# Performance work log

Measured on AMD Instinct MI355X. Metric: run time of the kernel, lower is better.

## Reference

```python
import jax, jax.numpy as jnp
import numpy as np

N, S, D, H = 2048, 16, 128, 8
EPS = 1e-5  # torch.nn.LayerNorm default eps


def setup_inputs() -> dict:
    key = jax.random.key(0)
    ks = jax.random.split(key, 3)
    return {
        "x": jax.random.normal(ks[0], (N, S, D), jnp.float32),
        "Wi": jax.random.normal(ks[1], (H, S, D, D), jnp.float32),
        "Wj": jax.random.normal(ks[2], (H, S, 2 * D, D), jnp.float32),
        "ln1_w": jnp.ones((S, D), jnp.float32),
        "ln1_b": jnp.zeros((S, D), jnp.float32),
        "prelu1_a": jnp.float32(0.25),  # torch PReLU default single param
        "ln2_w": jnp.ones((H, D), jnp.float32),
        "ln2_b": jnp.zeros((H, D), jnp.float32),
        "prelu2_a": jnp.float32(0.25),
    }


def _layernorm2(x, w, b):
    # LayerNorm over the last two dims (matches torch LayerNorm([A, B]))
    mu = jnp.mean(x, axis=(-2, -1), keepdims=True)
    var = jnp.var(x, axis=(-2, -1), keepdims=True)
    return (x - mu) * jax.lax.rsqrt(var + EPS) * w + b


def _prelu(x, a):
    return jnp.where(x >= 0, x, a * x)


def reference(x, Wi, Wj, ln1_w, ln1_b, prelu1_a, ln2_w, ln2_b, prelu2_a):
    n, s, d = x.shape
    h = Wi.shape[0]
    # sort descending along source dim
    idx = jnp.argsort(-x, axis=1)                      # [N,S,D] int
    x_sort = jnp.take_along_axis(x, idx, axis=1)       # [N,S,D]
    # pad with a zero row, take adjacent differences
    pad = jnp.concatenate([x_sort, jnp.zeros((n, 1, d), x.dtype)], axis=1)
    diff = pad[:, :-1, :] - pad[:, 1:, :]              # [N,S,D]
    # positional encoding: cumsum of 2^rank / 2^S
    enc = jnp.cumsum(jnp.exp2(idx.astype(x.dtype)), axis=1) / jnp.asarray(2.0 ** s, x.dtype)
    # per-head, per-source batched matmul with Wi
    se = jnp.einsum('bsd,hsdo->bhso', enc, Wi)         # [N,H,S,D]
    se = _prelu(_layernorm2(se, ln1_w, ln1_b), prelu1_a)  # Dropout in eval mode = identity
    cat = jnp.concatenate(
        [jnp.broadcast_to(diff[:, None, :, :], (n, h, s, d)), se], axis=-1
    )                                                  # [N,H,S,2D]
    out = jnp.einsum('bhsd,hsdo->bho', cat, Wj)        # [N,H,D]
    return _prelu(_layernorm2(out, ln2_w, ln2_b), prelu2_a)
```

## Files before the change

kernel.cpp:

```cpp
#include <hip/hip_runtime.h>

#define N_ 2048
#define S_ 16
#define D_ 128
#define H_ 8
#define EPS_ 1e-5f

typedef unsigned short ushortT;
typedef unsigned int uint32;
typedef __attribute__((ext_vector_type(8))) short short8;
typedef __attribute__((ext_vector_type(8))) unsigned short ushort8;
typedef __attribute__((ext_vector_type(4))) float f32x4;
typedef __attribute__((ext_vector_type(4))) unsigned int uint4v;
typedef __attribute__((ext_vector_type(8))) float float8;

__device__ __forceinline__ ushortT f2bf(float f) {
  union { float f; uint32 u; } c; c.f = f;
  uint32 u = c.u;
  u = (u + 0x7FFFu + ((u >> 16) & 1u)) >> 16;
  return (ushortT)u;
}
__device__ __forceinline__ float bf2f(ushortT b) {
  union { uint32 u; float f; } c; c.u = ((uint32)b) << 16;
  return c.f;
}

__global__ __launch_bounds__(256) void k_prep(const float* __restrict__ x,
                                              ushortT* __restrict__ enc_sw,
                                              ushortT* __restrict__ diff_sw) {
  int g = blockIdx.x * 256 + threadIdx.x;
  int n = g >> 7, d = g & 127;
  const float* xp = x + (size_t)n * (S_ * D_) + d;
  float v[S_];
#pragma unroll
  for (int s = 0; s < S_; ++s) v[s] = xp[s * D_];
  int r[S_];
#pragma unroll
  for (int i = 0; i < S_; ++i) {
    int ri = 0;
#pragma unroll
    for (int j = 0; j < S_; ++j)
      ri += ((v[j] > v[i]) || (v[j] == v[i] && j < i)) ? 1 : 0;
    r[i] = ri;
  }
  float xs[S_ + 1];
#pragma unroll
  for (int s = 0; s < S_; ++s) {
    float acc = 0.f;
#pragma unroll
    for (int i = 0; i < S_; ++i) acc += (r[i] == s) ? v[i] : 0.f;
    xs[s] = acc;
  }
  xs[S_] = 0.f;
  int btq = n >> 7, row = n & 127;
  int wv = row >> 5, ii = (row >> 4) & 1, l = row & 15;
  int kkm = d >> 5, lgm = (d >> 3) & 3, em = d & 7;
  int off_nd = (((kkm * 2 + ii) * 64) + (lgm * 16 + l)) * 8 + em;
  int pp = d >> 6, c8p = (d >> 3) & 7, ee = d & 7;
  int q = row * 8 + (c8p ^ (row & 7));
#pragma unroll
  for (int s = 0; s < S_; ++s) {
    uint32 mm = 0;
#pragma unroll
    for (int i = 0; i < S_; ++i) mm |= (r[i] <= s) ? (1u << i) : 0u;
    enc_sw[(size_t)((btq * 16 + s) * 4 + wv) * 4096 + off_nd] =
        f2bf((float)mm * (1.f / 65536.f));
    size_t idx = ((((size_t)(btq * 16 + s) * 2 + pp) * 1024) + q) * 8 + ee;
    diff_sw[idx] = f2bf(xs[s] - xs[s + 1]);
  }
}

__global__ __launch_bounds__(256) void k_castW(const float* __restrict__ Wi,
                                               const float* __restrict__ Wj,
                                               ushortT* __restrict__ Wit_sw,
                                               ushortT* __restrict__ Wjt_sw) {
  __shared__ ushortT tile[128 * 136];
  int bx = blockIdx.x;
  int t = threadIdx.x;
  if (bx < 128) {
    int hs = bx;
    const float* src = Wi + (size_t)hs * D_ * D_;
#pragma unroll 4
    for (int i = 0; i < 64; ++i) {
      int e = t + 256 * i;
      int dd = e >> 7, o = e & 127;
      tile[dd * 136 + o] = f2bf(src[e]);
    }
    __syncthreads();
    ushortT* dst = Wit_sw + (size_t)hs * 16384;
#pragma unroll
    for (int r8 = 0; r8 < 8; ++r8) {
      int qc = r8 * 256 + t;
      int o = qc >> 4;
      int cc = (qc & 15) ^ (o & 7);
      uint4v pk;
#pragma unroll
      for (int w = 0; w < 4; ++w) {
        int d0 = cc * 8 + w * 2;
        ushortT lo = tile[d0 * 136 + o];
        ushortT hi = tile[(d0 + 1) * 136 + o];
        pk[w] = (uint32)lo | ((uint32)hi << 16);
      }
      *(uint4v*)(dst + qc * 8) = pk;
    }
  } else {
    int hs = bx - 128;
    const float* src = Wj + (size_t)hs * 256 * D_;
    for (int half = 0; half < 2; ++half) {
      if (half) __syncthreads();
#pragma unroll 4
      for (int i = 0; i < 64; ++i) {
        int e = t + 256 * i;
        int dd = e >> 7, o = e & 127;
        tile[dd * 136 + o] = f2bf(src[half * 16384 + e]);
      }
      __syncthreads();
      ushortT* dstb = Wjt_sw + ((size_t)hs * 4 + half * 2) * 8192;
#pragma unroll
      for (int r8 = 0; r8 < 8; ++r8) {
        int cg = r8 * 256 + t;
        int pl = cg >> 10;
        int qc = cg & 1023;
        int o = qc >> 3;
        int c8 = (qc & 7) ^ (o & 7);
        int dl = pl * 64 + c8 * 8;
        uint4v pk;
#pragma unroll
        for (int w = 0; w < 4; ++w) {
          ushortT lo = tile[(dl + w * 2) * 136 + o];
          ushortT hi = tile[(dl + w * 2 + 1) * 136 + o];
          pk[w] = (uint32)lo | ((uint32)hi << 16);
        }
        *(uint4v*)(dstb + (size_t)pl * 8192 + qc * 8) = pk;
      }
    }
  }
}

__global__ __launch_bounds__(256, 3) void k_gemm1(const ushortT* __restrict__ enc_sw,
                                                  const ushortT* __restrict__ Wit_sw,
                                                  ushortT* __restrict__ se,
                                                  float* __restrict__ ssum,
                                                  float* __restrict__ ssq) {
  int bt = blockIdx.x, s = blockIdx.y, h = blockIdx.z;
  __shared__ ushortT Bs[128 * 132];
  int tid = threadIdx.x;
  int wave = tid >> 6, lane = tid & 63;
  int l15 = lane & 15, lg = lane >> 4;

  const ushortT* bsrc = Wit_sw + (size_t)(h * 16 + s) * 16384;
#pragma unroll
  for (int r8 = 0; r8 < 8; ++r8)
    __builtin_amdgcn_global_load_lds(
        (const __attribute__((address_space(1))) void*)(bsrc + (r8 * 256 + tid) * 8),
        (__attribute__((address_space(3))) void*)(Bs + (r8 * 256 + wave * 64) * 8),
        16, 0, 0);

  short8 afr[4][2];
  const ushortT* abase = enc_sw + ((size_t)(bt * 16 + s) * 4 + wave) * 4096;
#pragma unroll
  for (int kk = 0; kk < 4; ++kk)
#pragma unroll
    for (int i = 0; i < 2; ++i)
      afr[kk][i] = *(const short8*)(abase + ((kk * 2 + i) * 64 + lane) * 8);

  __syncthreads();

  f32x4 acc[2][8];
#pragma unroll
  for (int i = 0; i < 2; ++i)
#pragma unroll
    for (int j = 0; j < 8; ++j) acc[i][j] = (f32x4)(0.f);
#pragma unroll
  for (int kk = 0; kk < 4; ++kk) {
    int cc = kk * 4 + lg;
    short8 b[8];
#pragma unroll
    for (int j = 0; j < 8; ++j) {
      int row = j * 16 + l15;
      b[j] = *(const short8*)(Bs + (row * 16 + (cc ^ (row & 7))) * 8);
    }
#pragma unroll
    for (int i = 0; i < 2; ++i)
#pragma unroll
      for (int j = 0; j < 8; ++j)
        acc[i][j] = __builtin_amdgcn_mfma_f32_16x16x32_bf16(afr[kk][i], b[j], acc[i][j], 0, 0, 0);
  }
#pragma unroll
  for (int i = 0; i < 2; ++i)
#pragma unroll
    for (int rr = 0; rr < 4; ++rr) {
      int rloc = wave * 32 + i * 16 + lg * 4 + rr;
      int b_g = bt * 128 + rloc;
      float rs = 0.f, rq = 0.f;
#pragma unroll
      for (int j = 0; j < 8; ++j) {
        float val = acc[i][j][rr];
        rs += val; rq += val * val;
      }
#pragma unroll
      for (int m = 1; m <= 8; m <<= 1) {
        rs += __shfl_xor(rs, m);
        rq += __shfl_xor(rq, m);
      }
      if (l15 == 0) {
        ssum[((size_t)s * N_ + b_g) * H_ + h] = rs;
        ssq[((size_t)s * N_ + b_g) * H_ + h] = rq;
      }
    }
  __syncthreads();
#pragma unroll
  for (int i = 0; i < 2; ++i)
#pragma unroll
    for (int rr = 0; rr < 4; ++rr) {
      int row = wave * 32 + i * 16 + lg * 4 + rr;
      int sw = (row & 7) << 3;
#pragma unroll
      for (int j = 0; j < 8; ++j) {
        int o = j * 16 + l15;
        Bs[row * 132 + (o ^ sw)] = f2bf(acc[i][j][rr]);
      }
    }
  __syncthreads();
#pragma unroll
  for (int p = 0; p < 2; ++p) {
    int row = p * 64 + (tid >> 2);
    int sw = (row & 7) << 3;
    int b_g = bt * 128 + row;
    ushortT* dst = se + (((size_t)b_g * H_ + h) * S_ + s) * D_;
#pragma unroll
    for (int qq = 0; qq < 4; ++qq) {
      int o0 = (qq * 4 + (tid & 3)) * 8;
      *(uint4v*)(dst + o0) = *(const uint4v*)(Bs + row * 132 + (o0 ^ sw));
    }
  }
}

__global__ __launch_bounds__(256) void k_finalize(const float* __restrict__ ssum,
                                                  const float* __restrict__ ssq,
                                                  float* __restrict__ mr) {
  int t = blockIdx.x * 256 + threadIdx.x;
  float s1 = 0.f, s2 = 0.f;
#pragma unroll
  for (int s = 0; s < S_; ++s) {
    s1 += ssum[(size_t)s * (N_ * H_) + t];
    s2 += ssq[(size_t)s * (N_ * H_) + t];
  }
  float mu = s1 * (1.f / 2048.f);
  float var = s2 * (1.f / 2048.f) - mu * mu;
  float rstd = rsqrtf(var + EPS_);
  mr[t * 2] = rstd;
  mr[t * 2 + 1] = -mu * rstd;
}

#define GLDS_TILE(DST, SRC) do {                                              \
    const ushortT* sp_ = (SRC) + wave * 512 + lane * 8;                       \
    ushortT* dp_ = (DST) + wave * 512;                                        \
    _Pragma("unroll")                                                         \
    for (int i_ = 0; i_ < 4; ++i_)                                            \
      __builtin_amdgcn_global_load_lds(                                       \
          (const __attribute__((address_space(1))) void*)(sp_ + i_ * 2048),   \
          (__attribute__((address_space(3))) void*)(dp_ + i_ * 2048),         \
          16, 0, 0);                                                          \
  } while (0)

__global__ __launch_bounds__(256, 2) void k_gemm2(const ushortT* __restrict__ diff_sw,
                                                  const ushortT* __restrict__ se,
                                                  const ushortT* __restrict__ Wjt_sw,
                                                  const float* __restrict__ mr,
                                                  const float* __restrict__ ln1w,
                                                  const float* __restrict__ ln1b,
                                                  const float* __restrict__ pa1,
                                                  float* __restrict__ outp,
                                                  int scount) {
  int bt = blockIdx.x, sh = blockIdx.y, h = blockIdx.z;
  int s0 = sh * scount;
  __shared__ ushortT As[2][128 * 64];
  __shared__ ushortT Bs[2][128 * 64];
  int tid = threadIdx.x;
  int wave = tid >> 6, lane = tid & 63;
  int c8 = tid & 7, trow = tid >> 3;
  int swst = ((c8 ^ (trow & 7)) * 8);
  int l15 = lane & 15, lg = lane >> 4;
  int wm = wave >> 1, wn = wave & 1;
  float a1 = pa1[0];

  float rs_r[4], nm_r[4];
  uint32 aoff_s[4];
#pragma unroll
  for (int i = 0; i < 4; ++i) {
    int row = i * 32 + trow;
    int b_g = bt * 128 + row;
    rs_r[i] = mr[((size_t)b_g * H_ + h) * 2];
    nm_r[i] = mr[((size_t)b_g * H_ + h) * 2 + 1];
    aoff_s[i] = ((uint32)b_g * H_ + h) * (S_ * D_) + c8 * 8;
  }
  ushort8 raL[4], raH[4];
  f32x4 acc[4][4];
#pragma unroll
  for (int i = 0; i < 4; ++i)
#pragma unroll
    for (int j = 0; j < 4; ++j) acc[i][j] = (f32x4)(0.f);

#define COMPUTE(XBUF) do {                                                    \
    _Pragma("unroll")                                                         \
    for (int kk = 0; kk < 2; ++kk) {                                          \
      int cc = kk * 4 + lg;                                                   \
      short8 a[4], b[4];                                                      \
      _Pragma("unroll")                                                       \
      for (int i = 0; i < 4; ++i) {                                           \
        int row = wm * 64 + i * 16 + l15;                                     \
        a[i] = *(const short8*)(As[XBUF] + row * 64 + ((cc ^ (row & 7)) * 8));\
      }                                                                       \
      _Pragma("unroll")                                                       \
      for (int j = 0; j < 4; ++j) {                                           \
        int row = wn * 64 + j * 16 + l15;                                     \
        b[j] = *(const short8*)(Bs[XBUF] + row * 64 + ((cc ^ (row & 7)) * 8));\
      }                                                                       \
      _Pragma("unroll")                                                       \
      for (int i = 0; i < 4; ++i)                                             \
        _Pragma("unroll")                                                     \
        for (int j = 0; j < 4; ++j)                                           \
          acc[i][j] = __builtin_amdgcn_mfma_f32_16x16x32_bf16(a[i], b[j],     \
                                                              acc[i][j], 0, 0, 0); \
    } } while (0)

#define TRANSFORM_WRITE(RA, NXBUF, SS, HALF) do {                             \
    float8 w8 = *(const float8*)(ln1w + (SS) * D_ + (HALF) * 64 + c8 * 8);    \
    float8 b8 = *(const float8*)(ln1b + (SS) * D_ + (HALF) * 64 + c8 * 8);    \
    _Pragma("unroll")                                                         \
    for (int i = 0; i < 4; ++i) {                                             \
      int row = i * 32 + trow;                                                \
      float y[8];                                                             \
      _Pragma("unroll")                                                       \
      for (int e = 0; e < 8; ++e) {                                           \
        float f = bf2f((ushortT)RA[i][e]);                                    \
        float tt = fmaf(f, rs_r[i], nm_r[i]);                                 \
        float vv = fmaf(tt, w8[e], b8[e]);                                    \
        y[e] = fmaf(a1, fminf(vv, 0.f), fmaxf(vv, 0.f));                      \
      }                                                                       \
      uint4v pk;                                                              \
      _Pragma("unroll")                                                       \
      for (int q = 0; q < 4; ++q) {                                           \
        uint32 rpk;                                                           \
        asm("v_cvt_pk_bf16_f32 %0, %1, %2" : "=v"(rpk)                        \
            : "v"(y[2 * q]), "v"(y[2 * q + 1]));                              \
        pk[q] = rpk;                                                          \
      }                                                                       \
      *(uint4v*)(As[NXBUF] + row * 64 + swst) = pk;                           \
    } } while (0)

  GLDS_TILE(As[0], diff_sw + ((size_t)(bt * 16 + s0) * 2 + 0) * 8192);
  GLDS_TILE(Bs[0], Wjt_sw + ((size_t)(h * 16 + s0) * 4 + 0) * 8192);
  __syncthreads();

  for (int si = 0; si < scount; ++si) {
    int s = s0 + si;
    int sn = (s + 1 < S_) ? s + 1 : 0;
#pragma unroll
    for (int i = 0; i < 4; ++i)
      raL[i] = *(const ushort8*)(se + aoff_s[i] + s * D_);
    GLDS_TILE(As[1], diff_sw + ((size_t)(bt * 16 + s) * 2 + 1) * 8192);
    GLDS_TILE(Bs[1], Wjt_sw + ((size_t)(h * 16 + s) * 4 + 1) * 8192);
    COMPUTE(0);
    __syncthreads();
#pragma unroll
    for (int i = 0; i < 4; ++i)
      raH[i] = *(const ushort8*)(se + aoff_s[i] + s * D_ + 64);
    TRANSFORM_WRITE(raL, 0, s, 0);
    GLDS_TILE(Bs[0], Wjt_sw + ((size_t)(h * 16 + s) * 4 + 2) * 8192);
    COMPUTE(1);
    __syncthreads();
    TRANSFORM_WRITE(raH, 1, s, 1);
    GLDS_TILE(Bs[1], Wjt_sw + ((size_t)(h * 16 + s) * 4 + 3) * 8192);
    COMPUTE(0);
    __syncthreads();
    GLDS_TILE(As[0], diff_sw + ((size_t)(bt * 16 + sn) * 2 + 0) * 8192);
    GLDS_TILE(Bs[0], Wjt_sw + ((size_t)(h * 16 + sn) * 4 + 0) * 8192);
    COMPUTE(1);
    __syncthreads();
  }

#pragma unroll
  for (int i = 0; i < 4; ++i)
#pragma unroll
    for (int j = 0; j < 4; ++j)
#pragma unroll
      for (int rr = 0; rr < 4; ++rr) {
        int b_g = bt * 128 + wm * 64 + i * 16 + lg * 4 + rr;
        int o = wn * 64 + j * 16 + l15;
        outp[(((size_t)sh * N_ + b_g) * H_ + h) * D_ + o] = acc[i][j][rr];
      }
}

__global__ __launch_bounds__(256) void k_ln2(const float* __restrict__ outp,
                                             const float* __restrict__ ln2w,
                                             const float* __restrict__ ln2b,
                                             const float* __restrict__ pa2,
                                             float* __restrict__ out,
                                             int nsplit) {
  int b = blockIdx.x, t = threadIdx.x;
  __shared__ float red[8];
  __shared__ float stats[2];
  f32x4 v = (f32x4)(0.f);
  for (int p = 0; p < nsplit; ++p)
    v += *((const f32x4*)(outp + (size_t)p * (N_ * 1024) + (size_t)b * 1024) + t);
  float s1 = v[0] + v[1] + v[2] + v[3];
  float s2 = v[0] * v[0] + v[1] * v[1] + v[2] * v[2] + v[3] * v[3];
#pragma unroll
  for (int m = 1; m <= 32; m <<= 1) {
    s1 += __shfl_xor(s1, m);
    s2 += __shfl_xor(s2, m);
  }
  int wave = t >> 6, lane = t & 63;
  if (lane == 0) { red[wave] = s1; red[4 + wave] = s2; }
  __syncthreads();
  if (t == 0) {
    float S = red[0] + red[1] + red[2] + red[3];
    float Q = red[4] + red[5] + red[6] + red[7];
    float mu = S * (1.f / 1024.f);
    float var = Q * (1.f / 1024.f) - mu * mu;
    stats[0] = mu; stats[1] = rsqrtf(var + EPS_);
  }
  __syncthreads();
  float mu = stats[0], rstd = stats[1];
  float a2 = pa2[0];
  f32x4 wv = *((const f32x4*)ln2w + t);
  f32x4 bv = *((const f32x4*)ln2b + t);
  f32x4 r;
#pragma unroll
  for (int e = 0; e < 4; ++e) {
    float y = (v[e] - mu) * rstd * wv[e] + bv[e];
    r[e] = (y >= 0.f) ? y : a2 * y;
  }
  *((f32x4*)(out + (size_t)b * 1024) + t) = r;
}

extern "C" void kernel_launch(void* const* d_in, const int* in_sizes, int n_in,
                              void* d_out, int out_size, void* d_ws, size_t ws_size,
                              hipStream_t stream) {
  const float* x    = (const float*)d_in[0];
  const float* Wi   = (const float*)d_in[1];
  const float* Wj   = (const float*)d_in[2];
  const float* ln1w = (const float*)d_in[3];
  const float* ln1b = (const float*)d_in[4];
  const float* pa1  = (const float*)d_in[5];
  const float* ln2w = (const float*)d_in[6];
  const float* ln2b = (const float*)d_in[7];
  const float* pa2  = (const float*)d_in[8];
  char* ws = (char*)d_ws;
  ushortT* se      = (ushortT*)(ws + 0);
  ushortT* diff_sw = (ushortT*)(ws + 67108864);
  ushortT* Wjt_sw  = (ushortT*)(ws + 75497472);
  float*   outp    = (float*)(ws + 83886080);
  ushortT* enc_sw  = (ushortT*)(ws + 83886080);
  ushortT* Wit_sw  = (ushortT*)(ws + 92274688);
  float*   ssum    = (float*)(ws + 96468992);
  float*   ssq     = (float*)(ws + 97517568);
  float*   out     = (float*)d_out;

  int nsplit = (ws_size >= 117571584ull) ? 4 : 2;
  int scount = S_ / nsplit;
  float* mr = (float*)(ws + 83886080 + (size_t)nsplit * 8388608);

  hipLaunchKernelGGL(k_prep, dim3(1024), dim3(256), 0, stream, x, enc_sw, diff_sw);
  hipLaunchKernelGGL(k_castW, dim3(256), dim3(256), 0, stream, Wi, Wj, Wit_sw, Wjt_sw);
  hipLaunchKernelGGL(k_gemm1, dim3(16, 16, 8), dim3(256), 0, stream, enc_sw, Wit_sw, se, ssum, ssq);
  hipLaunchKernelGGL(k_finalize, dim3(64), dim3(256), 0, stream, ssum, ssq, mr);
  hipLaunchKernelGGL(k_gemm2, dim3(16, nsplit, 8), dim3(256), 0, stream, diff_sw, se, Wjt_sw, mr,
                     ln1w, ln1b, pa1, outp, scount);
  hipLaunchKernelGGL(k_ln2, dim3(2048), dim3(256), 0, stream, outp, ln2w, ln2b, pa2, out, nsplit);
}
```

Measured before the change: 188.4 us.

## Shrink gemm2 M-tile, fix split at two, add setprio and relayout enc

Halves the k_gemm2 block tile from 128 to 64 rows and fixes the S split at two, doubling the grid in x. It raises the occupancy hint to 3 blocks per CU and wraps the MFMA bursts in s_setprio. The enc fragment layout is permuted consistently between k_prep and k_gemm1, k_castW moves to 512-thread blocks, and the workspace is reorganised so k_ln2 always sums two partials. The smaller tile means more tiles per wave and less reuse of each B tile, in exchange for more parallelism and fewer partial-sum passes.

```diff
diff --git a/kernel.cpp b/kernel.cpp
--- a/kernel.cpp
+++ b/kernel.cpp
@@ -53,9 +53,9 @@
   }
   xs[S_] = 0.f;
   int btq = n >> 7, row = n & 127;
-  int wv = row >> 5, ii = (row >> 4) & 1, l = row & 15;
+  int wv = row >> 5, ii = (row >> 4) & 1, l15n = row & 15;
   int kkm = d >> 5, lgm = (d >> 3) & 3, em = d & 7;
-  int off_nd = (((kkm * 2 + ii) * 64) + (lgm * 16 + l)) * 8 + em;
+  int off_nd = (((kkm * 2 + ii) * 64) + (l15n * 4 + lgm)) * 8 + em;
   int pp = d >> 6, c8p = (d >> 3) & 7, ee = d & 7;
   int q = row * 8 + (c8p ^ (row & 7));
 #pragma unroll
@@ -70,7 +70,7 @@
   }
 }
 
-__global__ __launch_bounds__(256) void k_castW(const float* __restrict__ Wi,
+__global__ __launch_bounds__(512) void k_castW(const float* __restrict__ Wi,
                                                const float* __restrict__ Wj,
                                                ushortT* __restrict__ Wit_sw,
                                                ushortT* __restrict__ Wjt_sw) {
@@ -81,16 +81,16 @@
     int hs = bx;
     const float* src = Wi + (size_t)hs * D_ * D_;
 #pragma unroll 4
-    for (int i = 0; i < 64; ++i) {
-      int e = t + 256 * i;
+    for (int i = 0; i < 32; ++i) {
+      int e = t + 512 * i;
       int dd = e >> 7, o = e & 127;
       tile[dd * 136 + o] = f2bf(src[e]);
     }
     __syncthreads();
     ushortT* dst = Wit_sw + (size_t)hs * 16384;
 #pragma unroll
-    for (int r8 = 0; r8 < 8; ++r8) {
-      int qc = r8 * 256 + t;
+    for (int r8 = 0; r8 < 4; ++r8) {
+      int qc = r8 * 512 + t;
       int o = qc >> 4;
       int cc = (qc & 15) ^ (o & 7);
       uint4v pk;
@@ -109,16 +109,16 @@
     for (int half = 0; half < 2; ++half) {
       if (half) __syncthreads();
 #pragma unroll 4
-      for (int i = 0; i < 64; ++i) {
-        int e = t + 256 * i;
+      for (int i = 0; i < 32; ++i) {
+        int e = t + 512 * i;
         int dd = e >> 7, o = e & 127;
         tile[dd * 136 + o] = f2bf(src[half * 16384 + e]);
       }
       __syncthreads();
       ushortT* dstb = Wjt_sw + ((size_t)hs * 4 + half * 2) * 8192;
 #pragma unroll
-      for (int r8 = 0; r8 < 8; ++r8) {
-        int cg = r8 * 256 + t;
+      for (int r8 = 0; r8 < 4; ++r8) {
+        int cg = r8 * 512 + t;
         int pl = cg >> 10;
         int qc = cg & 1023;
         int o = qc >> 3;
@@ -162,7 +162,7 @@
   for (int kk = 0; kk < 4; ++kk)
 #pragma unroll
     for (int i = 0; i < 2; ++i)
-      afr[kk][i] = *(const short8*)(abase + ((kk * 2 + i) * 64 + lane) * 8);
+      afr[kk][i] = *(const short8*)(abase + (((kk * 2 + i) * 64) + (l15 * 4 + lg)) * 8);
 
   __syncthreads();
 
@@ -253,7 +253,7 @@
   mr[t * 2 + 1] = -mu * rstd;
 }
 
-#define GLDS_TILE(DST, SRC) do {                                              \
+#define GLDS_B(DST, SRC) do {                                                 \
     const ushortT* sp_ = (SRC) + wave * 512 + lane * 8;                       \
     ushortT* dp_ = (DST) + wave * 512;                                        \
     _Pragma("unroll")                                                         \
@@ -264,18 +264,28 @@
           16, 0, 0);                                                          \
   } while (0)
 
-__global__ __launch_bounds__(256, 2) void k_gemm2(const ushortT* __restrict__ diff_sw,
+#define GLDS_A(DST, SRC) do {                                                 \
+    const ushortT* sp_ = (SRC) + wave * 512 + lane * 8;                       \
+    ushortT* dp_ = (DST) + wave * 512;                                        \
+    _Pragma("unroll")                                                         \
+    for (int i_ = 0; i_ < 2; ++i_)                                            \
+      __builtin_amdgcn_global_load_lds(                                       \
+          (const __attribute__((address_space(1))) void*)(sp_ + i_ * 2048),   \
+          (__attribute__((address_space(3))) void*)(dp_ + i_ * 2048),         \
+          16, 0, 0);                                                          \
+  } while (0)
+
+__global__ __launch_bounds__(256, 3) void k_gemm2(const ushortT* __restrict__ diff_sw,
                                                   const ushortT* __restrict__ se,
                                                   const ushortT* __restrict__ Wjt_sw,
                                                   const float* __restrict__ mr,
                                                   const float* __restrict__ ln1w,
                                                   const float* __restrict__ ln1b,
                                                   const float* __restrict__ pa1,
-                                                  float* __restrict__ outp,
-                                                  int scount) {
-  int bt = blockIdx.x, sh = blockIdx.y, h = blockIdx.z;
-  int s0 = sh * scount;
-  __shared__ ushortT As[2][128 * 64];
+                                                  float* __restrict__ outp) {
+  int bt2 = blockIdx.x, sh = blockIdx.y, h = blockIdx.z;
+  int s0 = sh * 8;
+  __shared__ ushortT As[2][64 * 64];
   __shared__ ushortT Bs[2][128 * 64];
   int tid = threadIdx.x;
   int wave = tid >> 6, lane = tid & 63;
@@ -285,20 +295,21 @@
   int wm = wave >> 1, wn = wave & 1;
   float a1 = pa1[0];
 
-  float rs_r[4], nm_r[4];
-  uint32 aoff_s[4];
-#pragma unroll
-  for (int i = 0; i < 4; ++i) {
+  float rs_r[2], nm_r[2];
+  uint32 aoff_s[2];
+#pragma unroll
+  for (int i = 0; i < 2; ++i) {
     int row = i * 32 + trow;
-    int b_g = bt * 128 + row;
+    int b_g = bt2 * 64 + row;
     rs_r[i] = mr[((size_t)b_g * H_ + h) * 2];
     nm_r[i] = mr[((size_t)b_g * H_ + h) * 2 + 1];
     aoff_s[i] = ((uint32)b_g * H_ + h) * (S_ * D_) + c8 * 8;
   }
-  ushort8 raL[4], raH[4];
-  f32x4 acc[4][4];
-#pragma unroll
-  for (int i = 0; i < 4; ++i)
+  const ushortT* dbase = diff_sw + (size_t)(bt2 >> 1) * (S_ * 2 * 8192) + (bt2 & 1) * 4096;
+  ushort8 raL[2], raH[2];
+  f32x4 acc[2][4];
+#pragma unroll
+  for (int i = 0; i < 2; ++i)
 #pragma unroll
     for (int j = 0; j < 4; ++j) acc[i][j] = (f32x4)(0.f);
 
@@ -306,10 +317,10 @@
     _Pragma("unroll")                                                         \
     for (int kk = 0; kk < 2; ++kk) {                                          \
       int cc = kk * 4 + lg;                                                   \
-      short8 a[4], b[4];                                                      \
+      short8 a[2], b[4];                                                      \
       _Pragma("unroll")                                                       \
-      for (int i = 0; i < 4; ++i) {                                           \
-        int row = wm * 64 + i * 16 + l15;                                     \
+      for (int i = 0; i < 2; ++i) {                                           \
+        int row = wm * 32 + i * 16 + l15;                                     \
         a[i] = *(const short8*)(As[XBUF] + row * 64 + ((cc ^ (row & 7)) * 8));\
       }                                                                       \
       _Pragma("unroll")                                                       \
@@ -317,19 +328,21 @@
         int row = wn * 64 + j * 16 + l15;                                     \
         b[j] = *(const short8*)(Bs[XBUF] + row * 64 + ((cc ^ (row & 7)) * 8));\
       }                                                                       \
+      __builtin_amdgcn_s_setprio(1);                                          \
       _Pragma("unroll")                                                       \
-      for (int i = 0; i < 4; ++i)                                             \
+      for (int i = 0; i < 2; ++i)                                             \
         _Pragma("unroll")                                                     \
         for (int j = 0; j < 4; ++j)                                           \
           acc[i][j] = __builtin_amdgcn_mfma_f32_16x16x32_bf16(a[i], b[j],     \
                                                               acc[i][j], 0, 0, 0); \
+      __builtin_amdgcn_s_setprio(0);                                          \
     } } while (0)
 
 #define TRANSFORM_WRITE(RA, NXBUF, SS, HALF) do {                             \
     float8 w8 = *(const float8*)(ln1w + (SS) * D_ + (HALF) * 64 + c8 * 8);    \
     float8 b8 = *(const float8*)(ln1b + (SS) * D_ + (HALF) * 64 + c8 * 8);    \
     _Pragma("unroll")                                                         \
-    for (int i = 0; i < 4; ++i) {                                             \
+    for (int i = 0; i < 2; ++i) {                                             \
       int row = i * 32 + trow;                                                \
       float y[8];                                                             \
       _Pragma("unroll")                                                       \
@@ -350,44 +363,44 @@
       *(uint4v*)(As[NXBUF] + row * 64 + swst) = pk;                           \
     } } while (0)
 
-  GLDS_TILE(As[0], diff_sw + ((size_t)(bt * 16 + s0) * 2 + 0) * 8192);
-  GLDS_TILE(Bs[0], Wjt_sw + ((size_t)(h * 16 + s0) * 4 + 0) * 8192);
-  __syncthreads();
-
-  for (int si = 0; si < scount; ++si) {
+  GLDS_A(As[0], dbase + ((size_t)s0 * 2 + 0) * 8192);
+  GLDS_B(Bs[0], Wjt_sw + ((size_t)(h * 16 + s0) * 4 + 0) * 8192);
+  __syncthreads();
+
+  for (int si = 0; si < 8; ++si) {
     int s = s0 + si;
     int sn = (s + 1 < S_) ? s + 1 : 0;
 #pragma unroll
-    for (int i = 0; i < 4; ++i)
+    for (int i = 0; i < 2; ++i)
       raL[i] = *(const ushort8*)(se + aoff_s[i] + s * D_);
-    GLDS_TILE(As[1], diff_sw + ((size_t)(bt * 16 + s) * 2 + 1) * 8192);
-    GLDS_TILE(Bs[1], Wjt_sw + ((size_t)(h * 16 + s) * 4 + 1) * 8192);
+    GLDS_A(As[1], dbase + ((size_t)s * 2 + 1) * 8192);
+    GLDS_B(Bs[1], Wjt_sw + ((size_t)(h * 16 + s) * 4 + 1) * 8192);
     COMPUTE(0);
     __syncthreads();
 #pragma unroll
-    for (int i = 0; i < 4; ++i)
+    for (int i = 0; i < 2; ++i)
       raH[i] = *(const ushort8*)(se + aoff_s[i] + s * D_ + 64);
     TRANSFORM_WRITE(raL, 0, s, 0);
-    GLDS_TILE(Bs[0], Wjt_sw + ((size_t)(h * 16 + s) * 4 + 2) * 8192);
+    GLDS_B(Bs[0], Wjt_sw + ((size_t)(h * 16 + s) * 4 + 2) * 8192);
     COMPUTE(1);
     __syncthreads();
     TRANSFORM_WRITE(raH, 1, s, 1);
-    GLDS_TILE(Bs[1], Wjt_sw + ((size_t)(h * 16 + s) * 4 + 3) * 8192);
+    GLDS_B(Bs[1], Wjt_sw + ((size_t)(h * 16 + s) * 4 + 3) * 8192);
     COMPUTE(0);
     __syncthreads();
-    GLDS_TILE(As[0], diff_sw + ((size_t)(bt * 16 + sn) * 2 + 0) * 8192);
-    GLDS_TILE(Bs[0], Wjt_sw + ((size_t)(h * 16 + sn) * 4 + 0) * 8192);
+    GLDS_A(As[0], dbase + ((size_t)sn * 2 + 0) * 8192);
+    GLDS_B(Bs[0], Wjt_sw + ((size_t)(h * 16 + sn) * 4 + 0) * 8192);
     COMPUTE(1);
     __syncthreads();
   }
 
 #pragma unroll
-  for (int i = 0; i < 4; ++i)
+  for (int i = 0; i < 2; ++i)
 #pragma unroll
     for (int j = 0; j < 4; ++j)
 #pragma unroll
       for (int rr = 0; rr < 4; ++rr) {
-        int b_g = bt * 128 + wm * 64 + i * 16 + lg * 4 + rr;
+        int b_g = bt2 * 64 + wm * 32 + i * 16 + lg * 4 + rr;
         int o = wn * 64 + j * 16 + l15;
         outp[(((size_t)sh * N_ + b_g) * H_ + h) * D_ + o] = acc[i][j][rr];
       }
@@ -397,14 +410,12 @@
                                              const float* __restrict__ ln2w,
                                              const float* __restrict__ ln2b,
                                              const float* __restrict__ pa2,
-                                             float* __restrict__ out,
-                                             int nsplit) {
+                                             float* __restrict__ out) {
   int b = blockIdx.x, t = threadIdx.x;
   __shared__ float red[8];
   __shared__ float stats[2];
-  f32x4 v = (f32x4)(0.f);
-  for (int p = 0; p < nsplit; ++p)
-    v += *((const f32x4*)(outp + (size_t)p * (N_ * 1024) + (size_t)b * 1024) + t);
+  f32x4 v = *((const f32x4*)(outp + (size_t)b * 1024) + t) +
+            *((const f32x4*)(outp + (size_t)N_ * 1024 + (size_t)b * 1024) + t);
   float s1 = v[0] + v[1] + v[2] + v[3];
   float s2 = v[0] * v[0] + v[1] * v[1] + v[2] * v[2] + v[3] * v[3];
 #pragma unroll
@@ -453,21 +464,18 @@
   ushortT* diff_sw = (ushortT*)(ws + 67108864);
   ushortT* Wjt_sw  = (ushortT*)(ws + 75497472);
   float*   outp    = (float*)(ws + 83886080);
-  ushortT* enc_sw  = (ushortT*)(ws + 83886080);
-  ushortT* Wit_sw  = (ushortT*)(ws + 92274688);
-  float*   ssum    = (float*)(ws + 96468992);
-  float*   ssq     = (float*)(ws + 97517568);
+  ushortT* enc_sw  = (ushortT*)(ws + 100663296);
+  ushortT* Wit_sw  = (ushortT*)(ws + 109051904);
+  float*   ssum    = (float*)(ws + 113246208);
+  float*   ssq     = (float*)(ws + 114294784);
+  float*   mr      = (float*)(ws + 115343360);
   float*   out     = (float*)d_out;
 
-  int nsplit = (ws_size >= 117571584ull) ? 4 : 2;
-  int scount = S_ / nsplit;
-  float* mr = (float*)(ws + 83886080 + (size_t)nsplit * 8388608);
-
   hipLaunchKernelGGL(k_prep, dim3(1024), dim3(256), 0, stream, x, enc_sw, diff_sw);
-  hipLaunchKernelGGL(k_castW, dim3(256), dim3(256), 0, stream, Wi, Wj, Wit_sw, Wjt_sw);
+  hipLaunchKernelGGL(k_castW, dim3(256), dim3(512), 0, stream, Wi, Wj, Wit_sw, Wjt_sw);
   hipLaunchKernelGGL(k_gemm1, dim3(16, 16, 8), dim3(256), 0, stream, enc_sw, Wit_sw, se, ssum, ssq);
   hipLaunchKernelGGL(k_finalize, dim3(64), dim3(256), 0, stream, ssum, ssq, mr);
-  hipLaunchKernelGGL(k_gemm2, dim3(16, nsplit, 8), dim3(256), 0, stream, diff_sw, se, Wjt_sw, mr,
-                     ln1w, ln1b, pa1, outp, scount);
-  hipLaunchKernelGGL(k_ln2, dim3(2048), dim3(256), 0, stream, outp, ln2w, ln2b, pa2, out, nsplit);
-}
+  hipLaunchKernelGGL(k_gemm2, dim3(32, 2, 8), dim3(256), 0, stream, diff_sw, se, Wjt_sw, mr,
+                     ln1w, ln1b, pa1, outp);
+  hipLaunchKernelGGL(k_ln2, dim3(2048), dim3(256), 0, stream, outp, ln2w, ln2b, pa2, out);
+}
```

Result: faster. 183.4 us (-2.7%).
